# Kernel tuning notes

Hardware: AMD Instinct MI355X
Metric: run time of the kernel (lower is better)

The kernel has to match this reference:

```python
import jax, jax.numpy as jnp
import numpy as np

N = 50000      # nodes
E = 800000     # directed edges (before self loops)
F_IN = 2613    # raw feature dim (nn.Linear(2613, 256))
D = 256        # hidden dim, heads = 1
BN_EPS = 1e-5
NEG_SLOPE = 0.2  # PyG GATConv default negative_slope


def setup_inputs() -> dict:
    key = jax.random.key(0)
    ks = jax.random.split(key, 12)

    def glorot(k, shape):
        s = (6.0 / (shape[0] + shape[-1])) ** 0.5
        return jax.random.uniform(k, shape, jnp.float32, -s, s)

    zeros = lambda: jnp.zeros((D,), jnp.float32)
    ones = lambda: jnp.ones((D,), jnp.float32)
    return {
        "x": jax.random.normal(ks[0], (N, F_IN), dtype=jnp.float32),
        "edges": jax.random.randint(ks[1], (2, E), 0, N, dtype=jnp.int32),
        "W1": glorot(ks[2], (F_IN, D)), "b1": zeros(),
        "W2": glorot(ks[3], (D, D)), "b2": zeros(),
        "W3": glorot(ks[4], (D, D)), "b3": zeros(),
        "g1": ones(), "be1": zeros(),
        "g2": ones(), "be2": zeros(),
        "g3": ones(), "be3": zeros(),
        "Wg1": glorot(ks[5], (D, D)),
        "att_src1": glorot(ks[6], (D,)), "att_dst1": glorot(ks[7], (D,)),
        "bg1": zeros(), "g4": ones(), "be4": zeros(),
        "Wg2": glorot(ks[8], (D, D)),
        "att_src2": glorot(ks[9], (D,)), "att_dst2": glorot(ks[10], (D,)),
        "bg2": zeros(), "g5": ones(), "be5": zeros(),
    }


def batch_norm(h, gamma, beta):
    # BatchNorm1d in training mode: batch statistics over the node axis
    mu = h.mean(axis=0)
    var = h.var(axis=0)
    return (h - mu) * jax.lax.rsqrt(var + BN_EPS) * gamma + beta


def gat_conv(h, W, att_src, att_dst, bias, src, dst):
    # PyG GATConv, heads=1: shared linear for src/dst, additive attention,
    # leaky_relu scores, softmax over incoming edges per destination node.
    xl = h @ W                              # [N, D]
    a_src = xl @ att_src                    # [N]
    a_dst = xl @ att_dst                    # [N]
    e = jax.nn.leaky_relu(a_src[src] + a_dst[dst], NEG_SLOPE)  # [E+N]
    m = jax.ops.segment_max(jax.lax.stop_gradient(e), dst, num_segments=N)
    w = jnp.exp(e - m[dst])
    denom = jax.ops.segment_sum(w, dst, num_segments=N)
    alpha = w / (denom[dst] + 1e-16)        # [E+N]
    out = jax.ops.segment_sum(alpha[:, None] * xl[src], dst, num_segments=N)
    return out + bias


def reference(x, edges, W1, b1, W2, b2, W3, b3, g1, be1, g2, be2, g3, be3,
              Wg1, att_src1, att_dst1, bg1, g4, be4,
              Wg2, att_src2, att_dst2, bg2, g5, be5):
    # PyG GATConv default add_self_loops=True
    loops = jnp.arange(N, dtype=edges.dtype)
    src = jnp.concatenate([edges[0], loops])
    dst = jnp.concatenate([edges[1], loops])

    h = jax.nn.elu(batch_norm(x @ W1 + b1, g1, be1))
    h = jax.nn.elu(batch_norm(h @ W2 + b2, g2, be2))
    h = jax.nn.elu(batch_norm(h @ W3 + b3, g3, be3))
    h = gat_conv(h, Wg1, att_src1, att_dst1, bg1, src, dst)
    h = jax.nn.elu(batch_norm(h, g4, be4))
    h = gat_conv(h, Wg2, att_src2, att_dst2, bg2, src, dst)
    h = jax.nn.elu(batch_norm(h, g5, be5))
    return h
```

## Files before the change

kernel.cpp:

```cpp
#include <hip/hip_runtime.h>

#define DEV __device__ __forceinline__

typedef __attribute__((ext_vector_type(4))) float f32x4;
typedef __attribute__((ext_vector_type(8))) short short8;

DEV float bf2f(unsigned short u) {
    union { unsigned int i; float f; } c;
    c.i = ((unsigned int)u) << 16;
    return c.f;
}
DEV unsigned short f2bf(float f) {
    union { float f; unsigned int i; } c;
    c.f = f;
    unsigned int u = c.i;
    u += 0x7FFFu + ((u >> 16) & 1u);
    return (unsigned short)(u >> 16);
}

template<bool A_F32, bool OUT_BF16, bool STATS>
__launch_bounds__(512)
__global__ void gemm_k(const void* __restrict__ Aptr,
                       const unsigned short* __restrict__ Bt,
                       void* __restrict__ Cptr,
                       float* __restrict__ st,
                       int M, int lda, int ldb, int ksteps)
{
    __shared__ __align__(16) unsigned short As[2][128 * 64];
    __shared__ __align__(16) unsigned short Bs[2][256 * 64];
    const int t    = threadIdx.x;
    const int wid  = t >> 6;
    const int lane = t & 63;
    const int wr   = wid >> 2;
    const int wc   = wid & 3;
    const int m0   = blockIdx.x * 128;

    const float* Af          = (const float*)Aptr;
    const unsigned short* Ab = (const unsigned short*)Aptr;
    const size_t maxoff = (size_t)M * (size_t)lda - 4;

    f32x4 acc[4][4] = {};
    float ar0[16], ar1[16];

    auto stageB = [&](int buf, int ks) {
        const int k0 = ks * 64;
        #pragma unroll
        for (int is = 0; is < 4; ++is) {
            const int rbase = wid * 32 + is * 8;
            const int rr  = rbase + (lane >> 3);
            const int csw = (lane & 7) ^ (rr & 7);
            __builtin_amdgcn_global_load_lds(
                (const __attribute__((address_space(1))) void*)(Bt + (size_t)rr * ldb + k0 + csw * 8),
                (__attribute__((address_space(3))) void*)(&Bs[buf][rbase * 64]),
                16, 0, 0);
        }
    };
    auto stageAb = [&](int buf, int ks) {
        const int k0 = ks * 64;
        #pragma unroll
        for (int is = 0; is < 2; ++is) {
            const int rbase = wid * 16 + is * 8;
            const int rr  = rbase + (lane >> 3);
            const int csw = (lane & 7) ^ (rr & 7);
            __builtin_amdgcn_global_load_lds(
                (const __attribute__((address_space(1))) void*)(Ab + (size_t)(m0 + rr) * lda + k0 + csw * 8),
                (__attribute__((address_space(3))) void*)(&As[buf][rbase * 64]),
                16, 0, 0);
        }
    };
    auto loadAf = [&](int ks, float (&ar)[16]) {
        const int k0 = ks * 64;
        #pragma unroll
        for (int i = 0; i < 4; ++i) {
            const int tt  = t + i * 512;
            const int row = tt >> 4;
            const int cg  = tt & 15;
            size_t off = (size_t)(m0 + row) * lda + (k0 + cg * 4);
            off = off < maxoff ? off : maxoff;
            *(f32x4*)&ar[i * 4] = *(const f32x4*)(Af + off);
        }
    };
    auto writeAf = [&](int buf, float (&ar)[16]) {
        #pragma unroll
        for (int i = 0; i < 4; ++i) {
            const int tt  = t + i * 512;
            const int row = tt >> 4;
            const int cg  = tt & 15;
            uint2 pk;
            pk.x = (unsigned int)f2bf(ar[i * 4 + 0]) | ((unsigned int)f2bf(ar[i * 4 + 1]) << 16);
            pk.y = (unsigned int)f2bf(ar[i * 4 + 2]) | ((unsigned int)f2bf(ar[i * 4 + 3]) << 16);
            *(uint2*)&As[buf][row * 64 + ((((cg >> 1) ^ (row & 7)) << 3) | ((cg & 1) << 2))] = pk;
        }
    };
    auto compute = [&](int buf) {
        #pragma unroll
        for (int kk = 0; kk < 2; ++kk) {
            short8 af[4], bfr[4];
            #pragma unroll
            for (int mi = 0; mi < 4; ++mi) {
                const int r   = wr * 64 + mi * 16 + (lane & 15);
                const int csw = (kk * 4 + (lane >> 4)) ^ (r & 7);
                af[mi] = *(const short8*)(&As[buf][r * 64 + csw * 8]);
            }
            #pragma unroll
            for (int ni = 0; ni < 4; ++ni) {
                const int r   = wc * 64 + ni * 16 + (lane & 15);
                const int csw = (kk * 4 + (lane >> 4)) ^ (r & 7);
                bfr[ni] = *(const short8*)(&Bs[buf][r * 64 + csw * 8]);
            }
            #pragma unroll
            for (int mi = 0; mi < 4; ++mi)
                #pragma unroll
                for (int ni = 0; ni < 4; ++ni)
                    acc[mi][ni] = __builtin_amdgcn_mfma_f32_16x16x32_bf16(
                        af[mi], bfr[ni], acc[mi][ni], 0, 0, 0);
        }
    };

    if constexpr (A_F32) loadAf(0, ar0); else stageAb(0, 0);
    stageB(0, 0);
    __builtin_amdgcn_sched_barrier(0);
    if constexpr (A_F32) loadAf(1, ar1); else stageAb(1, 1);
    stageB(1, 1);
    if constexpr (A_F32) {
        asm volatile("s_waitcnt vmcnt(8)" ::: "memory");
        __builtin_amdgcn_sched_barrier(0);
        writeAf(0, ar0);
        asm volatile("s_waitcnt lgkmcnt(0)" ::: "memory");
    } else {
        asm volatile("s_waitcnt vmcnt(6)" ::: "memory");
    }
    __builtin_amdgcn_sched_barrier(0);
    __builtin_amdgcn_s_barrier();
    __builtin_amdgcn_sched_barrier(0);

    int cur = 0;
    for (int k = 0; k < ksteps; ++k) {
        compute(cur);
        if (k + 1 >= ksteps) break;
        __builtin_amdgcn_sched_barrier(0);
        __builtin_amdgcn_s_barrier();
        __builtin_amdgcn_sched_barrier(0);
        if (k + 2 < ksteps) {
            if constexpr (A_F32) {
                if (k & 1) loadAf(k + 2, ar1); else loadAf(k + 2, ar0);
            } else {
                stageAb(cur, k + 2);
            }
            stageB(cur, k + 2);
            if constexpr (A_F32)
                asm volatile("s_waitcnt vmcnt(8)" ::: "memory");
            else
                asm volatile("s_waitcnt vmcnt(6)" ::: "memory");
        } else {
            asm volatile("s_waitcnt vmcnt(0)" ::: "memory");
        }
        __builtin_amdgcn_sched_barrier(0);
        if constexpr (A_F32) {
            if (k & 1) writeAf(cur ^ 1, ar0); else writeAf(cur ^ 1, ar1);
            asm volatile("s_waitcnt lgkmcnt(0)" ::: "memory");
            __builtin_amdgcn_sched_barrier(0);
        }
        __builtin_amdgcn_s_barrier();
        __builtin_amdgcn_sched_barrier(0);
        cur ^= 1;
    }

    #pragma unroll
    for (int mi = 0; mi < 4; ++mi) {
        #pragma unroll
        for (int ni = 0; ni < 4; ++ni) {
            const int col = wc * 64 + ni * 16 + (lane & 15);
            #pragma unroll
            for (int rg = 0; rg < 4; ++rg) {
                const int m = m0 + wr * 64 + mi * 16 + (lane >> 4) * 4 + rg;
                if (m < M) {
                    if constexpr (OUT_BF16)
                        ((unsigned short*)Cptr)[(size_t)m * 256 + col] = f2bf(acc[mi][ni][rg]);
                    else
                        ((float*)Cptr)[(size_t)m * 256 + col] = acc[mi][ni][rg];
                }
            }
        }
    }
    if constexpr (STATS) {
        #pragma unroll
        for (int ni = 0; ni < 4; ++ni) {
            float s = 0.f, q = 0.f;
            #pragma unroll
            for (int mi = 0; mi < 4; ++mi)
                #pragma unroll
                for (int rg = 0; rg < 4; ++rg) {
                    const int m = m0 + wr * 64 + mi * 16 + (lane >> 4) * 4 + rg;
                    const float v = (m < M) ? acc[mi][ni][rg] : 0.f;
                    s += v; q += v * v;
                }
            s += __shfl_xor(s, 16); q += __shfl_xor(q, 16);
            s += __shfl_xor(s, 32); q += __shfl_xor(q, 32);
            if (lane < 16) {
                const int col = wc * 64 + ni * 16 + lane;
                atomicAdd(&st[col], s);
                atomicAdd(&st[256 + col], q);
            }
        }
    }
}

__global__ void wtrans_k(const float* __restrict__ W, unsigned short* __restrict__ WT,
                         int K, int ldb) {
    int total = 256 * ldb;
    for (int idx = blockIdx.x * blockDim.x + threadIdx.x; idx < total;
         idx += gridDim.x * blockDim.x) {
        int n = idx / ldb, k = idx - n * ldb;
        WT[idx] = f2bf(k < K ? W[(size_t)k * 256 + n] : 0.f);
    }
}

__global__ void colstats_k(const float* __restrict__ h, float* st, int total4) {
    const int gid    = blockIdx.x * 256 + threadIdx.x;
    const int stride = gridDim.x * 256;
    float4 s = {0.f, 0.f, 0.f, 0.f}, q = {0.f, 0.f, 0.f, 0.f};
    for (int i = gid; i < total4; i += stride) {
        float4 v = ((const float4*)h)[i];
        s.x += v.x; s.y += v.y; s.z += v.z; s.w += v.w;
        q.x += v.x * v.x; q.y += v.y * v.y; q.z += v.z * v.z; q.w += v.w * v.w;
    }
    __shared__ float red[2][4][64][4];
    const int wid = threadIdx.x >> 6, lane = threadIdx.x & 63;
    *(float4*)&red[0][wid][lane][0] = s;
    *(float4*)&red[1][wid][lane][0] = q;
    __syncthreads();
    if (wid == 0) {
        float4 s0 = *(float4*)&red[0][0][lane][0];
        float4 q0 = *(float4*)&red[1][0][lane][0];
        #pragma unroll
        for (int w = 1; w < 4; ++w) {
            float4 sw = *(float4*)&red[0][w][lane][0];
            float4 qw = *(float4*)&red[1][w][lane][0];
            s0.x += sw.x; s0.y += sw.y; s0.z += sw.z; s0.w += sw.w;
            q0.x += qw.x; q0.y += qw.y; q0.z += qw.z; q0.w += qw.w;
        }
        atomicAdd(&st[lane * 4 + 0], s0.x);
        atomicAdd(&st[lane * 4 + 1], s0.y);
        atomicAdd(&st[lane * 4 + 2], s0.z);
        atomicAdd(&st[lane * 4 + 3], s0.w);
        atomicAdd(&st[256 + lane * 4 + 0], q0.x);
        atomicAdd(&st[256 + lane * 4 + 1], q0.y);
        atomicAdd(&st[256 + lane * 4 + 2], q0.z);
        atomicAdd(&st[256 + lane * 4 + 3], q0.w);
    }
}

__global__ void bnfinal_k(const float* __restrict__ st, const float* __restrict__ g,
                          const float* __restrict__ be, float* __restrict__ ss, float invN) {
    int c = threadIdx.x;
    float mu  = st[c] * invN;
    float var = st[256 + c] * invN - mu * mu;
    float sc  = g[c] * rsqrtf(var + 1e-5f);
    ss[c]       = sc;
    ss[256 + c] = be[c] - mu * sc;
}

template<bool OUT_BF16>
__global__ void bnelu_k(const float* h, const float* ss, void* outp, int total4) {
    for (int i = blockIdx.x * blockDim.x + threadIdx.x; i < total4;
         i += gridDim.x * blockDim.x) {
        float4 v = ((const float4*)h)[i];
        int c = (i << 2) & 255;
        float4 y;
        y.x = fmaf(v.x, ss[c + 0], ss[256 + c + 0]);
        y.y = fmaf(v.y, ss[c + 1], ss[256 + c + 1]);
        y.z = fmaf(v.z, ss[c + 2], ss[256 + c + 2]);
        y.w = fmaf(v.w, ss[c + 3], ss[256 + c + 3]);
        y.x = y.x > 0.f ? y.x : expm1f(y.x);
        y.y = y.y > 0.f ? y.y : expm1f(y.y);
        y.z = y.z > 0.f ? y.z : expm1f(y.z);
        y.w = y.w > 0.f ? y.w : expm1f(y.w);
        if (OUT_BF16) {
            ushort4 o;
            o.x = f2bf(y.x); o.y = f2bf(y.y); o.z = f2bf(y.z); o.w = f2bf(y.w);
            ((ushort4*)outp)[i] = o;
        } else {
            ((float4*)outp)[i] = y;
        }
    }
}

__global__ void adot_k(const unsigned short* __restrict__ xl, const float* __restrict__ as_,
                       const float* __restrict__ ad_, float* __restrict__ a_src,
                       float* __restrict__ a_dst, int N) {
    int w = (blockIdx.x * blockDim.x + threadIdx.x) >> 6;
    int lane = threadIdx.x & 63;
    if (w >= N) return;
    ushort4 v = *(const ushort4*)(xl + (size_t)w * 256 + lane * 4);
    float4 s4 = *(const float4*)(as_ + lane * 4);
    float4 d4 = *(const float4*)(ad_ + lane * 4);
    float x0 = bf2f(v.x), x1 = bf2f(v.y), x2 = bf2f(v.z), x3 = bf2f(v.w);
    float ps = x0 * s4.x + x1 * s4.y + x2 * s4.z + x3 * s4.w;
    float pd = x0 * d4.x + x1 * d4.y + x2 * d4.z + x3 * d4.w;
    #pragma unroll
    for (int off = 32; off; off >>= 1) {
        ps += __shfl_xor(ps, off);
        pd += __shfl_xor(pd, off);
    }
    if (lane == 0) { a_src[w] = ps; a_dst[w] = pd; }
}

__global__ void gat_k(const unsigned short* __restrict__ xl, const float* __restrict__ a_src,
                      const float* __restrict__ a_dst, const int* __restrict__ csr,
                      const int* __restrict__ indptr, float* __restrict__ out, int N) {
    int d = (blockIdx.x * blockDim.x + threadIdx.x) >> 6;
    int lane = threadIdx.x & 63;
    if (d >= N) return;
    int beg = indptr[d], end = indptr[d + 1];
    float adst = a_dst[d];
    float mx = -1e30f;
    for (int i = beg + lane; i < end; i += 64) {
        float e = a_src[csr[i]] + adst;
        e = e > 0.f ? e : 0.2f * e;
        mx = fmaxf(mx, e);
    }
    #pragma unroll
    for (int off = 32; off; off >>= 1) mx = fmaxf(mx, __shfl_xor(mx, off));
    float sm = 0.f;
    for (int i = beg + lane; i < end; i += 64) {
        float e = a_src[csr[i]] + adst;
        e = e > 0.f ? e : 0.2f * e;
        sm += __expf(e - mx);
    }
    #pragma unroll
    for (int off = 32; off; off >>= 1) sm += __shfl_xor(sm, off);
    float inv = 1.f / (sm + 1e-16f);
    float4 acc = {0.f, 0.f, 0.f, 0.f};
    for (int i = beg; i < end; ++i) {
        int s = csr[i];
        float e = a_src[s] + adst;
        e = e > 0.f ? e : 0.2f * e;
        float al = __expf(e - mx) * inv;
        ushort4 v = *(const ushort4*)(xl + (size_t)s * 256 + lane * 4);
        acc.x += al * bf2f(v.x);
        acc.y += al * bf2f(v.y);
        acc.z += al * bf2f(v.z);
        acc.w += al * bf2f(v.w);
    }
    *(float4*)(out + (size_t)d * 256 + lane * 4) = acc;
}

__global__ void hist_k(const int* __restrict__ edges, int* deg, int E, int N) {
    int total = E + N;
    for (int i = blockIdx.x * blockDim.x + threadIdx.x; i < total;
         i += gridDim.x * blockDim.x) {
        int dd = (i < E) ? edges[E + i] : (i - E);
        atomicAdd(&deg[dd], 1);
    }
}

__global__ void scan1_k(const int* __restrict__ deg, int* iscan, int* bsum, int N) {
    int i = blockIdx.x * 256 + threadIdx.x;
    int lane = threadIdx.x & 63, wid = threadIdx.x >> 6;
    int v = (i < N) ? deg[i] : 0;
    #pragma unroll
    for (int off = 1; off < 64; off <<= 1) {
        int u = __shfl_up(v, off);
        if (lane >= off) v += u;
    }
    __shared__ int wsum[4];
    if (lane == 63) wsum[wid] = v;
    __syncthreads();
    #pragma unroll
    for (int w = 0; w < 3; ++w) if (wid > w) v += wsum[w];
    if (i < N) iscan[i] = v;
    if (threadIdx.x == 255) bsum[blockIdx.x] = v;
}

__global__ void scan2_k(int* bsum, int nb) {
    int t = threadIdx.x;
    int lane = t & 63, wid = t >> 6;
    int v = (t < nb) ? bsum[t] : 0;
    int orig = v;
    #pragma unroll
    for (int off = 1; off < 64; off <<= 1) {
        int u = __shfl_up(v, off);
        if (lane >= off) v += u;
    }
    __shared__ int wsum[4];
    if (lane == 63) wsum[wid] = v;
    __syncthreads();
    #pragma unroll
    for (int w = 0; w < 3; ++w) if (wid > w) v += wsum[w];
    if (t < nb) bsum[t] = v - orig;
}

__global__ void scan3_k(const int* __restrict__ iscan, const int* __restrict__ boff,
                        int* indptr, int N) {
    int i = blockIdx.x * 256 + threadIdx.x;
    if (i < N) indptr[i + 1] = iscan[i] + boff[blockIdx.x];
    if (i == 0) indptr[0] = 0;
}

__global__ void copy_k(const int* __restrict__ a, int* b, int N) {
    for (int i = blockIdx.x * blockDim.x + threadIdx.x; i < N;
         i += gridDim.x * blockDim.x) b[i] = a[i];
}

__global__ void scatter_k(const int* __restrict__ edges, int* pos, int* csr, int E, int N) {
    int total = E + N;
    for (int i = blockIdx.x * blockDim.x + threadIdx.x; i < total;
         i += gridDim.x * blockDim.x) {
        int s  = (i < E) ? edges[i]     : (i - E);
        int dd = (i < E) ? edges[E + i] : (i - E);
        int slot = atomicAdd(&pos[dd], 1);
        csr[slot] = s;
    }
}

extern "C" void kernel_launch(void* const* d_in, const int* in_sizes, int n_in,
                              void* d_out, int out_size, void* d_ws, size_t ws_size,
                              hipStream_t stream) {
    const float* x     = (const float*)d_in[0];
    const int*   edges = (const int*)d_in[1];
    const float* W1 = (const float*)d_in[2];
    const float* W2 = (const float*)d_in[4];
    const float* W3 = (const float*)d_in[6];
    const float* g1 = (const float*)d_in[8],  *be1 = (const float*)d_in[9];
    const float* g2 = (const float*)d_in[10], *be2 = (const float*)d_in[11];
    const float* g3 = (const float*)d_in[12], *be3 = (const float*)d_in[13];
    const float* Wg1 = (const float*)d_in[14];
    const float* as1 = (const float*)d_in[15], *ad1 = (const float*)d_in[16];
    const float* g4 = (const float*)d_in[18], *be4 = (const float*)d_in[19];
    const float* Wg2 = (const float*)d_in[20];
    const float* as2 = (const float*)d_in[21], *ad2 = (const float*)d_in[22];
    const float* g5 = (const float*)d_in[24], *be5 = (const float*)d_in[25];

    const int N    = out_size / 256;
    const int K1   = in_sizes[0] / N;
    const int E    = in_sizes[1] / 2;
    const int Etot = E + N;
    const int ks1  = (K1 + 63) / 64;
    const int ldb1 = ks1 * 64;

    char* p = (char*)d_ws;
    auto alloc = [&](size_t bytes) {
        char* r = p;
        p += (bytes + 255) & ~(size_t)255;
        return r;
    };
    unsigned short* W1T  = (unsigned short*)alloc((size_t)256 * ldb1 * 2);
    unsigned short* W2T  = (unsigned short*)alloc(256 * 256 * 2);
    unsigned short* W3T  = (unsigned short*)alloc(256 * 256 * 2);
    unsigned short* Wg1T = (unsigned short*)alloc(256 * 256 * 2);
    unsigned short* Wg2T = (unsigned short*)alloc(256 * 256 * 2);
    unsigned short* hn   = (unsigned short*)alloc((size_t)N * 256 * 2);
    unsigned short* xl   = (unsigned short*)alloc((size_t)N * 256 * 2);
    float* a_src  = (float*)alloc((size_t)N * 4);
    float* a_dst  = (float*)alloc((size_t)N * 4);
    int*   deg    = (int*)alloc((size_t)N * 4);
    int*   iscan  = (int*)alloc((size_t)N * 4);
    int*   bsum   = (int*)alloc(1024);
    int*   indptr = (int*)alloc((size_t)(N + 1) * 4);
    int*   pos    = (int*)alloc((size_t)N * 4);
    int*   csr    = (int*)alloc((size_t)Etot * 4);
    float* st     = (float*)alloc(512 * 4);
    float* ss     = (float*)alloc(512 * 4);
    (void)alloc(65536);
    float* out = (float*)d_out;

    const int nb = (N + 255) / 256;
    const int eg = (Etot + 255) / 256;
    const int gb = (N + 127) / 128;
    const int t4 = N * 64;
    const int bg4 = (t4 + 255) / 256;

    hipMemsetAsync(deg, 0, (size_t)N * 4, stream);
    hist_k<<<eg, 256, 0, stream>>>(edges, deg, E, N);
    scan1_k<<<nb, 256, 0, stream>>>(deg, iscan, bsum, N);
    scan2_k<<<1, 256, 0, stream>>>(bsum, nb);
    scan3_k<<<nb, 256, 0, stream>>>(iscan, bsum, indptr, N);
    copy_k<<<nb, 256, 0, stream>>>(indptr, pos, N);
    scatter_k<<<eg, 256, 0, stream>>>(edges, pos, csr, E, N);

    wtrans_k<<<(256 * ldb1 + 255) / 256, 256, 0, stream>>>(W1, W1T, K1, ldb1);
    wtrans_k<<<256, 256, 0, stream>>>(W2, W2T, 256, 256);
    wtrans_k<<<256, 256, 0, stream>>>(W3, W3T, 256, 256);
    wtrans_k<<<256, 256, 0, stream>>>(Wg1, Wg1T, 256, 256);
    wtrans_k<<<256, 256, 0, stream>>>(Wg2, Wg2T, 256, 256);

    const float invN = 1.f / (float)N;

    hipMemsetAsync(st, 0, 2048, stream);
    gemm_k<true, false, true><<<gb, 512, 0, stream>>>(x, W1T, out, st, N, K1, ldb1, ks1);
    bnfinal_k<<<1, 256, 0, stream>>>(st, g1, be1, ss, invN);
    bnelu_k<true><<<bg4, 256, 0, stream>>>(out, ss, hn, t4);

    hipMemsetAsync(st, 0, 2048, stream);
    gemm_k<false, false, true><<<gb, 512, 0, stream>>>(hn, W2T, out, st, N, 256, 256, 4);
    bnfinal_k<<<1, 256, 0, stream>>>(st, g2, be2, ss, invN);
    bnelu_k<true><<<bg4, 256, 0, stream>>>(out, ss, hn, t4);

    hipMemsetAsync(st, 0, 2048, stream);
    gemm_k<false, false, true><<<gb, 512, 0, stream>>>(hn, W3T, out, st, N, 256, 256, 4);
    bnfinal_k<<<1, 256, 0, stream>>>(st, g3, be3, ss, invN);
    bnelu_k<true><<<bg4, 256, 0, stream>>>(out, ss, hn, t4);

    gemm_k<false, true, false><<<gb, 512, 0, stream>>>(hn, Wg1T, xl, st, N, 256, 256, 4);
    adot_k<<<(N + 3) / 4, 256, 0, stream>>>(xl, as1, ad1, a_src, a_dst, N);
    gat_k<<<(N + 3) / 4, 256, 0, stream>>>(xl, a_src, a_dst, csr, indptr, out, N);
    hipMemsetAsync(st, 0, 2048, stream);
    colstats_k<<<1024, 256, 0, stream>>>(out, st, t4);
    bnfinal_k<<<1, 256, 0, stream>>>(st, g4, be4, ss, invN);
    bnelu_k<true><<<bg4, 256, 0, stream>>>(out, ss, hn, t4);

    gemm_k<false, true, false><<<gb, 512, 0, stream>>>(hn, Wg2T, xl, st, N, 256, 256, 4);
    adot_k<<<(N + 3) / 4, 256, 0, stream>>>(xl, as2, ad2, a_src, a_dst, N);
    gat_k<<<(N + 3) / 4, 256, 0, stream>>>(xl, a_src, a_dst, csr, indptr, out, N);
    hipMemsetAsync(st, 0, 2048, stream);
    colstats_k<<<1024, 256, 0, stream>>>(out, st, t4);
    bnfinal_k<<<1, 256, 0, stream>>>(st, g5, be5, ss, invN);
    bnelu_k<false><<<bg4, 256, 0, stream>>>(out, ss, out, t4);
}
```

Measured before the change: 1.026 ms.

## Pre-convert fp32 input to padded bf16 and unroll GAT aggregation by four

Adds a separate pass that converts the 50000x2613 fp32 input to a padded bf16 buffer, so the first GEMM can stage A with async global-to-LDS loads instead of register loads plus in-kernel conversion. The extra pass reads the fp32 matrix once and writes a bf16 copy, adding traffic in exchange for a simpler, better-pipelined GEMM. Separately, the GAT aggregation loop now processes four edges per iteration with independent accumulators, raising memory-level parallelism for the gathers.

```diff
diff --git a/kernel.cpp b/kernel.cpp
--- a/kernel.cpp
+++ b/kernel.cpp
@@ -18,9 +18,40 @@
     return (unsigned short)(u >> 16);
 }
 
-template<bool A_F32, bool OUT_BF16, bool STATS>
+__global__ void cvt_pad_k(const float* __restrict__ x, unsigned short* __restrict__ xb,
+                          int M, int K, int Kp) {
+    const int gpr = Kp >> 3;
+    const long long total = (long long)M * gpr;
+    for (long long g = blockIdx.x * (long long)blockDim.x + threadIdx.x; g < total;
+         g += (long long)gridDim.x * blockDim.x) {
+        const int row = (int)(g / gpr);
+        const int c8  = (int)(g - (long long)row * gpr);
+        const int k0  = c8 * 8;
+        const float* src = x + (size_t)row * K + k0;
+        unsigned int w[4];
+        if (k0 + 8 <= K) {
+            f32x4 v0 = *(const f32x4*)(src);
+            f32x4 v1 = *(const f32x4*)(src + 4);
+            w[0] = (unsigned int)f2bf(v0[0]) | ((unsigned int)f2bf(v0[1]) << 16);
+            w[1] = (unsigned int)f2bf(v0[2]) | ((unsigned int)f2bf(v0[3]) << 16);
+            w[2] = (unsigned int)f2bf(v1[0]) | ((unsigned int)f2bf(v1[1]) << 16);
+            w[3] = (unsigned int)f2bf(v1[2]) | ((unsigned int)f2bf(v1[3]) << 16);
+        } else {
+            unsigned short o[8];
+            #pragma unroll
+            for (int j = 0; j < 8; ++j) o[j] = (k0 + j < K) ? f2bf(src[j]) : (unsigned short)0;
+            w[0] = o[0] | ((unsigned int)o[1] << 16);
+            w[1] = o[2] | ((unsigned int)o[3] << 16);
+            w[2] = o[4] | ((unsigned int)o[5] << 16);
+            w[3] = o[6] | ((unsigned int)o[7] << 16);
+        }
+        *(uint4*)(xb + (size_t)row * Kp + k0) = *(uint4*)w;
+    }
+}
+
+template<bool OUT_BF16, bool STATS>
 __launch_bounds__(512)
-__global__ void gemm_k(const void* __restrict__ Aptr,
+__global__ void gemm_k(const unsigned short* __restrict__ A,
                        const unsigned short* __restrict__ Bt,
                        void* __restrict__ Cptr,
                        float* __restrict__ st,
@@ -35,12 +66,7 @@
     const int wc   = wid & 3;
     const int m0   = blockIdx.x * 128;
 
-    const float* Af          = (const float*)Aptr;
-    const unsigned short* Ab = (const unsigned short*)Aptr;
-    const size_t maxoff = (size_t)M * (size_t)lda - 4;
-
     f32x4 acc[4][4] = {};
-    float ar0[16], ar1[16];
 
     auto stageB = [&](int buf, int ks) {
         const int k0 = ks * 64;
@@ -55,7 +81,7 @@
                 16, 0, 0);
         }
     };
-    auto stageAb = [&](int buf, int ks) {
+    auto stageA = [&](int buf, int ks) {
         const int k0 = ks * 64;
         #pragma unroll
         for (int is = 0; is < 2; ++is) {
@@ -63,33 +89,9 @@
             const int rr  = rbase + (lane >> 3);
             const int csw = (lane & 7) ^ (rr & 7);
             __builtin_amdgcn_global_load_lds(
-                (const __attribute__((address_space(1))) void*)(Ab + (size_t)(m0 + rr) * lda + k0 + csw * 8),
+                (const __attribute__((address_space(1))) void*)(A + (size_t)(m0 + rr) * lda + k0 + csw * 8),
                 (__attribute__((address_space(3))) void*)(&As[buf][rbase * 64]),
                 16, 0, 0);
-        }
-    };
-    auto loadAf = [&](int ks, float (&ar)[16]) {
-        const int k0 = ks * 64;
-        #pragma unroll
-        for (int i = 0; i < 4; ++i) {
-            const int tt  = t + i * 512;
-            const int row = tt >> 4;
-            const int cg  = tt & 15;
-            size_t off = (size_t)(m0 + row) * lda + (k0 + cg * 4);
-            off = off < maxoff ? off : maxoff;
-            *(f32x4*)&ar[i * 4] = *(const f32x4*)(Af + off);
-        }
-    };
-    auto writeAf = [&](int buf, float (&ar)[16]) {
-        #pragma unroll
-        for (int i = 0; i < 4; ++i) {
-            const int tt  = t + i * 512;
-            const int row = tt >> 4;
-            const int cg  = tt & 15;
-            uint2 pk;
-            pk.x = (unsigned int)f2bf(ar[i * 4 + 0]) | ((unsigned int)f2bf(ar[i * 4 + 1]) << 16);
-            pk.y = (unsigned int)f2bf(ar[i * 4 + 2]) | ((unsigned int)f2bf(ar[i * 4 + 3]) << 16);
-            *(uint2*)&As[buf][row * 64 + ((((cg >> 1) ^ (row & 7)) << 3) | ((cg & 1) << 2))] = pk;
         }
     };
     auto compute = [&](int buf) {
@@ -117,19 +119,10 @@
         }
     };
 
-    if constexpr (A_F32) loadAf(0, ar0); else stageAb(0, 0);
-    stageB(0, 0);
+    stageA(0, 0); stageB(0, 0);
     __builtin_amdgcn_sched_barrier(0);
-    if constexpr (A_F32) loadAf(1, ar1); else stageAb(1, 1);
-    stageB(1, 1);
-    if constexpr (A_F32) {
-        asm volatile("s_waitcnt vmcnt(8)" ::: "memory");
-        __builtin_amdgcn_sched_barrier(0);
-        writeAf(0, ar0);
-        asm volatile("s_waitcnt lgkmcnt(0)" ::: "memory");
-    } else {
-        asm volatile("s_waitcnt vmcnt(6)" ::: "memory");
-    }
+    stageA(1, 1); stageB(1, 1);
+    asm volatile("s_waitcnt vmcnt(6)" ::: "memory");
     __builtin_amdgcn_sched_barrier(0);
     __builtin_amdgcn_s_barrier();
     __builtin_amdgcn_sched_barrier(0);
@@ -142,25 +135,13 @@
         __builtin_amdgcn_s_barrier();
         __builtin_amdgcn_sched_barrier(0);
         if (k + 2 < ksteps) {
-            if constexpr (A_F32) {
-                if (k & 1) loadAf(k + 2, ar1); else loadAf(k + 2, ar0);
-            } else {
-                stageAb(cur, k + 2);
-            }
+            stageA(cur, k + 2);
             stageB(cur, k + 2);
-            if constexpr (A_F32)
-                asm volatile("s_waitcnt vmcnt(8)" ::: "memory");
-            else
-                asm volatile("s_waitcnt vmcnt(6)" ::: "memory");
+            asm volatile("s_waitcnt vmcnt(6)" ::: "memory");
         } else {
             asm volatile("s_waitcnt vmcnt(0)" ::: "memory");
         }
         __builtin_amdgcn_sched_barrier(0);
-        if constexpr (A_F32) {
-            if (k & 1) writeAf(cur ^ 1, ar0); else writeAf(cur ^ 1, ar1);
-            asm volatile("s_waitcnt lgkmcnt(0)" ::: "memory");
-            __builtin_amdgcn_sched_barrier(0);
-        }
         __builtin_amdgcn_s_barrier();
         __builtin_amdgcn_sched_barrier(0);
         cur ^= 1;
@@ -306,6 +287,8 @@
     if (lane == 0) { a_src[w] = ps; a_dst[w] = pd; }
 }
 
+DEV float lrelu(float e) { return e > 0.f ? e : 0.2f * e; }
+
 __global__ void gat_k(const unsigned short* __restrict__ xl, const float* __restrict__ a_src,
                       const float* __restrict__ a_dst, const int* __restrict__ csr,
                       const int* __restrict__ indptr, float* __restrict__ out, int N) {
@@ -315,35 +298,46 @@
     int beg = indptr[d], end = indptr[d + 1];
     float adst = a_dst[d];
     float mx = -1e30f;
-    for (int i = beg + lane; i < end; i += 64) {
-        float e = a_src[csr[i]] + adst;
-        e = e > 0.f ? e : 0.2f * e;
-        mx = fmaxf(mx, e);
-    }
+    for (int i = beg + lane; i < end; i += 64)
+        mx = fmaxf(mx, lrelu(a_src[csr[i]] + adst));
     #pragma unroll
     for (int off = 32; off; off >>= 1) mx = fmaxf(mx, __shfl_xor(mx, off));
     float sm = 0.f;
-    for (int i = beg + lane; i < end; i += 64) {
-        float e = a_src[csr[i]] + adst;
-        e = e > 0.f ? e : 0.2f * e;
-        sm += __expf(e - mx);
-    }
+    for (int i = beg + lane; i < end; i += 64)
+        sm += __expf(lrelu(a_src[csr[i]] + adst) - mx);
     #pragma unroll
     for (int off = 32; off; off >>= 1) sm += __shfl_xor(sm, off);
     float inv = 1.f / (sm + 1e-16f);
-    float4 acc = {0.f, 0.f, 0.f, 0.f};
-    for (int i = beg; i < end; ++i) {
+
+    float4 A0 = {0,0,0,0}, A1 = {0,0,0,0}, A2 = {0,0,0,0}, A3 = {0,0,0,0};
+    int i = beg;
+    for (; i + 4 <= end; i += 4) {
+        int s0 = csr[i], s1 = csr[i+1], s2 = csr[i+2], s3 = csr[i+3];
+        float w0 = __expf(lrelu(a_src[s0] + adst) - mx) * inv;
+        float w1 = __expf(lrelu(a_src[s1] + adst) - mx) * inv;
+        float w2 = __expf(lrelu(a_src[s2] + adst) - mx) * inv;
+        float w3 = __expf(lrelu(a_src[s3] + adst) - mx) * inv;
+        ushort4 v0 = *(const ushort4*)(xl + (size_t)s0 * 256 + lane * 4);
+        ushort4 v1 = *(const ushort4*)(xl + (size_t)s1 * 256 + lane * 4);
+        ushort4 v2 = *(const ushort4*)(xl + (size_t)s2 * 256 + lane * 4);
+        ushort4 v3 = *(const ushort4*)(xl + (size_t)s3 * 256 + lane * 4);
+        A0.x += w0 * bf2f(v0.x); A0.y += w0 * bf2f(v0.y); A0.z += w0 * bf2f(v0.z); A0.w += w0 * bf2f(v0.w);
+        A1.x += w1 * bf2f(v1.x); A1.y += w1 * bf2f(v1.y); A1.z += w1 * bf2f(v1.z); A1.w += w1 * bf2f(v1.w);
+        A2.x += w2 * bf2f(v2.x); A2.y += w2 * bf2f(v2.y); A2.z += w2 * bf2f(v2.z); A2.w += w2 * bf2f(v2.w);
+        A3.x += w3 * bf2f(v3.x); A3.y += w3 * bf2f(v3.y); A3.z += w3 * bf2f(v3.z); A3.w += w3 * bf2f(v3.w);
+    }
+    for (; i < end; ++i) {
         int s = csr[i];
-        float e = a_src[s] + adst;
-        e = e > 0.f ? e : 0.2f * e;
-        float al = __expf(e - mx) * inv;
+        float w = __expf(lrelu(a_src[s] + adst) - mx) * inv;
         ushort4 v = *(const ushort4*)(xl + (size_t)s * 256 + lane * 4);
-        acc.x += al * bf2f(v.x);
-        acc.y += al * bf2f(v.y);
-        acc.z += al * bf2f(v.z);
-        acc.w += al * bf2f(v.w);
-    }
-    *(float4*)(out + (size_t)d * 256 + lane * 4) = acc;
+        A0.x += w * bf2f(v.x); A0.y += w * bf2f(v.y);
+        A0.z += w * bf2f(v.z); A0.w += w * bf2f(v.w);
+    }
+    A0.x += A1.x + A2.x + A3.x;
+    A0.y += A1.y + A2.y + A3.y;
+    A0.z += A1.z + A2.z + A3.z;
+    A0.w += A1.w + A2.w + A3.w;
+    *(float4*)(out + (size_t)d * 256 + lane * 4) = A0;
 }
 
 __global__ void hist_k(const int* __restrict__ edges, int* deg, int E, int N) {
@@ -450,6 +444,7 @@
     unsigned short* W3T  = (unsigned short*)alloc(256 * 256 * 2);
     unsigned short* Wg1T = (unsigned short*)alloc(256 * 256 * 2);
     unsigned short* Wg2T = (unsigned short*)alloc(256 * 256 * 2);
+    unsigned short* xb   = (unsigned short*)alloc((size_t)N * ldb1 * 2);
     unsigned short* hn   = (unsigned short*)alloc((size_t)N * 256 * 2);
     unsigned short* xl   = (unsigned short*)alloc((size_t)N * 256 * 2);
     float* a_src  = (float*)alloc((size_t)N * 4);
@@ -462,7 +457,7 @@
     int*   csr    = (int*)alloc((size_t)Etot * 4);
     float* st     = (float*)alloc(512 * 4);
     float* ss     = (float*)alloc(512 * 4);
-    (void)alloc(65536);
+    (void)alloc(1 << 19);
     float* out = (float*)d_out;
 
     const int nb = (N + 255) / 256;
@@ -484,25 +479,26 @@
     wtrans_k<<<256, 256, 0, stream>>>(W3, W3T, 256, 256);
     wtrans_k<<<256, 256, 0, stream>>>(Wg1, Wg1T, 256, 256);
     wtrans_k<<<256, 256, 0, stream>>>(Wg2, Wg2T, 256, 256);
+    cvt_pad_k<<<2048, 256, 0, stream>>>(x, xb, N, K1, ldb1);
 
     const float invN = 1.f / (float)N;
 
     hipMemsetAsync(st, 0, 2048, stream);
-    gemm_k<true, false, true><<<gb, 512, 0, stream>>>(x, W1T, out, st, N, K1, ldb1, ks1);
+    gemm_k<false, true><<<gb, 512, 0, stream>>>(xb, W1T, out, st, N, ldb1, ldb1, ks1);
     bnfinal_k<<<1, 256, 0, stream>>>(st, g1, be1, ss, invN);
     bnelu_k<true><<<bg4, 256, 0, stream>>>(out, ss, hn, t4);
 
     hipMemsetAsync(st, 0, 2048, stream);
-    gemm_k<false, false, true><<<gb, 512, 0, stream>>>(hn, W2T, out, st, N, 256, 256, 4);
+    gemm_k<false, true><<<gb, 512, 0, stream>>>(hn, W2T, out, st, N, 256, 256, 4);
     bnfinal_k<<<1, 256, 0, stream>>>(st, g2, be2, ss, invN);
     bnelu_k<true><<<bg4, 256, 0, stream>>>(out, ss, hn, t4);
 
     hipMemsetAsync(st, 0, 2048, stream);
-    gemm_k<false, false, true><<<gb, 512, 0, stream>>>(hn, W3T, out, st, N, 256, 256, 4);
+    gemm_k<false, true><<<gb, 512, 0, stream>>>(hn, W3T, out, st, N, 256, 256, 4);
     bnfinal_k<<<1, 256, 0, stream>>>(st, g3, be3, ss, invN);
     bnelu_k<true><<<bg4, 256, 0, stream>>>(out, ss, hn, t4);
 
-    gemm_k<false, true, false><<<gb, 512, 0, stream>>>(hn, Wg1T, xl, st, N, 256, 256, 4);
+    gemm_k<true, false><<<gb, 512, 0, stream>>>(hn, Wg1T, xl, st, N, 256, 256, 4);
     adot_k<<<(N + 3) / 4, 256, 0, stream>>>(xl, as1, ad1, a_src, a_dst, N);
     gat_k<<<(N + 3) / 4, 256, 0, stream>>>(xl, a_src, a_dst, csr, indptr, out, N);
     hipMemsetAsync(st, 0, 2048, stream);
@@ -510,7 +506,7 @@
     bnfinal_k<<<1, 256, 0, stream>>>(st, g4, be4, ss, invN);
     bnelu_k<true><<<bg4, 256, 0, stream>>>(out, ss, hn, t4);
 
-    gemm_k<false, true, false><<<gb, 512, 0, stream>>>(hn, Wg2T, xl, st, N, 256, 256, 4);
+    gemm_k<true, false><<<gb, 512, 0, stream>>>(hn, Wg2T, xl, st, N, 256, 256, 4);
     adot_k<<<(N + 3) / 4, 256, 0, stream>>>(xl, as2, ad2, a_src, a_dst, N);
     gat_k<<<(N + 3) / 4, 256, 0, stream>>>(xl, a_src, a_dst, csr, indptr, out, N);
     hipMemsetAsync(st, 0, 2048, stream);
```

Result: faster. 998.3 us (-2.7%).
